# Kernel tuning notes

Hardware: AMD Instinct MI355X
Metric: run time of the kernel (lower is better)

The kernel has to match this reference:

```python
import jax, jax.numpy as jnp
import numpy as np

NUM_HEADS = 12
ROPE_THETA = 10000.0


def rope_angles(hd, end_x, end_y):
    # axial 2D rope angles, shape (L, hd//2); first hd//4 from x-coord, next hd//4 from y-coord
    f = 1.0 / (ROPE_THETA ** (np.arange(0, hd, 4)[: hd // 4].astype(np.float32) / hd))
    t = np.arange(end_x * end_y)
    tx = (t % end_x).astype(np.float32)
    ty = (t // end_x).astype(np.float32)
    ang = np.concatenate([np.outer(tx, f), np.outer(ty, f)], axis=-1)
    return jnp.asarray(ang, dtype=jnp.float32)


def apply_rope(q, ang):
    # q: (B, nH, L, hd); complex multiply on adjacent pairs
    cos, sin = jnp.cos(ang), jnp.sin(ang)  # (L, hd//2)
    qr = q.reshape(*q.shape[:-1], -1, 2)
    a, b = qr[..., 0], qr[..., 1]
    return jnp.stack([a * cos - b * sin, a * sin + b * cos], axis=-1).reshape(q.shape)


def setup_inputs() -> dict:
    key = jax.random.key(0)
    ks = jax.random.split(key, 7)
    dim, H, W, B = 768, 32, 32, 8
    hd = dim // NUM_HEADS
    return {
        "x": jax.random.normal(ks[0], (B, H, W, dim), jnp.float32),
        "qkv_w": jax.random.normal(ks[1], (3 * dim, dim), jnp.float32) * 0.02,
        "qkv_b": jax.random.normal(ks[2], (3 * dim,), jnp.float32) * 0.02,
        "proj_w": jax.random.normal(ks[3], (dim, dim), jnp.float32) * 0.02,
        "proj_b": jax.random.normal(ks[4], (dim,), jnp.float32) * 0.02,
        "rel_pos_h": jax.random.normal(ks[5], (2 * H - 1, hd), jnp.float32) * 0.02,
        "rel_pos_w": jax.random.normal(ks[6], (2 * W - 1, hd), jnp.float32) * 0.02,
    }


def reference(x, qkv_w, qkv_b, proj_w, proj_b, rel_pos_h, rel_pos_w):
    B, H, W, dim = x.shape
    nH = NUM_HEADS
    hd = dim // nH
    L = H * W
    qkv = jnp.einsum("blc,dc->bld", x.reshape(B, L, dim), qkv_w) + qkv_b
    qkv = qkv.reshape(B, L, 3, nH, hd)
    q = qkv[:, :, 0].transpose(0, 2, 1, 3)  # (B, nH, L, hd)
    k = qkv[:, :, 1].transpose(0, 2, 1, 3)
    v = qkv[:, :, 2].transpose(0, 2, 1, 3)
    # 2D rope (applied to both q and k)
    ang = rope_angles(hd, H, W)
    q = apply_rope(q, ang)
    k = apply_rope(k, ang)
    # relative position bias: equivalent math of concat_rel_pos(rescale=True) + SDPA
    # effective scores = (q.k)/sqrt(hd) + rel_h + rel_w
    rc = jnp.arange(H)[:, None] - jnp.arange(W)[None, :] + (H - 1)  # (H, W)
    Rh = rel_pos_h[rc]  # (H, K_h, hd)
    Rw = rel_pos_w[rc]  # (W, K_w, hd)
    rq = q.reshape(B, nH, H, W, hd)
    rel_h = jnp.einsum("bnhwc,hkc->bnhwk", rq, Rh)  # (B, nH, H, W, K_h)
    rel_w = jnp.einsum("bnhwc,wkc->bnhwk", rq, Rw)  # (B, nH, H, W, K_w)
    scores = jnp.einsum("bnqc,bnkc->bnqk", q, k) / jnp.sqrt(jnp.float32(hd))
    scores = scores.reshape(B, nH, H, W, H, W) + rel_h[..., :, None] + rel_w[..., None, :]
    attn = jax.nn.softmax(scores.reshape(B, nH, L, L), axis=-1)
    out = jnp.einsum("bnqk,bnkc->bnqc", attn, v)  # (B, nH, L, hd)
    out = out.transpose(0, 2, 1, 3).reshape(B, H, W, dim)
    return jnp.einsum("bhwc,dc->bhwd", out, proj_w) + proj_b
```

## Files before the change

kernel.cpp:

```cpp
#include <hip/hip_runtime.h>


typedef unsigned short u16;
typedef __attribute__((ext_vector_type(8))) __bf16 bf16x8;
typedef __attribute__((ext_vector_type(4))) float f32x4;
typedef __attribute__((address_space(1))) const unsigned int gu32;
typedef __attribute__((address_space(3))) unsigned int lu32;

#define LOG2E 1.4426950408889634f

__device__ __forceinline__ float b2f(u16 u) {
    unsigned int i = ((unsigned int)u) << 16;
    float f; __builtin_memcpy(&f, &i, 4); return f;
}
__device__ __forceinline__ u16 f2b(float f) {
    unsigned int x; __builtin_memcpy(&x, &f, 4);
    x += 0x7fffu + ((x >> 16) & 1u);
    return (u16)(x >> 16);
}

#define LDT 72

__global__ void detect_dtype(const u16* __restrict__ x, int* __restrict__ flag)
{
    if (threadIdx.x == 0 && blockIdx.x == 0) {
        float mx = 0.f;
        for (int i = 0; i < 128; i++) {
            float v = fabsf(b2f(x[i]));
            if (!(v <= 1e30f)) v = 1e30f;
            mx = fmaxf(mx, v);
        }
        *flag = (mx > 1e4f) ? 1 : 0;
    }
}

struct CvtArgs {
    const void* src[7];
    u16*        dst[7];
    int         n[7];
    float       sc[7];
};

__global__ __launch_bounds__(256) void convert_all(CvtArgs a, const int* __restrict__ flag)
{
    const int fl = *flag;
    const int g = blockIdx.x * 256 + threadIdx.x;
    const int stride = gridDim.x * 256;
    #pragma unroll 1
    for (int s = 0; s < 7; s++) {
        const int n = a.n[s];
        const float sc = a.sc[s];
        const float* fs = (const float*)a.src[s];
        const u16*  hs = (const u16*)a.src[s];
        u16* d = a.dst[s];
        for (int i = g; i < n; i += stride) {
            float v = fl ? fs[i] : b2f(hs[i]);
            d[i] = f2b(v * sc);
        }
    }
}

template <int EPI>
__global__ __launch_bounds__(256) void gemm128(
    const u16* __restrict__ A, const u16* __restrict__ Bw,
    const u16* __restrict__ bias, void* __restrict__ Cout,
    const int* __restrict__ flag, u16* __restrict__ qkvT, int N, int K)
{
    __shared__ __align__(16) u16 smem[16384];
    u16* lA = smem;
    u16* lB = smem + 8192;
    u16* ct = smem;
    const int tid = threadIdx.x;
    const int m0 = blockIdx.x * 128, n0 = blockIdx.y * 128;
    const int wave = tid >> 6, lane = tid & 63;
    const int wm = (wave & 1) * 64, wn = (wave >> 1) * 64;
    const int lm = lane & 15, lq = lane >> 4;
    const int srow = lane >> 3;
    const int sgcol = ((lane & 7) ^ (srow & 7)) * 8;
    const int sw0 = (lq ^ (lm & 7)) * 8;
    const int sw1 = ((lq + 4) ^ (lm & 7)) * 8;
    f32x4 acc[4][4] = {};
    for (int k0 = 0; k0 < K; k0 += 64) {
        if (k0) __syncthreads();
        #pragma unroll
        for (int c4 = 0; c4 < 4; c4++) {
            const int c = wave * 4 + c4;
            const int row = c * 8 + srow;
            __builtin_amdgcn_global_load_lds(
                (gu32*)(A + (size_t)(m0 + row) * K + k0 + sgcol),
                (lu32*)&lA[c * 512], 16, 0, 0);
            __builtin_amdgcn_global_load_lds(
                (gu32*)(Bw + (size_t)(n0 + row) * K + k0 + sgcol),
                (lu32*)&lB[c * 512], 16, 0, 0);
        }
        __syncthreads();
        #pragma unroll
        for (int ks = 0; ks < 64; ks += 32) {
            const int sw = ks ? sw1 : sw0;
            bf16x8 af[4], bfr[4];
            #pragma unroll
            for (int i = 0; i < 4; i++) af[i]  = *(const bf16x8*)&lA[(wm + i * 16 + lm) * 64 + sw];
            #pragma unroll
            for (int j = 0; j < 4; j++) bfr[j] = *(const bf16x8*)&lB[(wn + j * 16 + lm) * 64 + sw];
            #pragma unroll
            for (int i = 0; i < 4; i++)
                #pragma unroll
                for (int j = 0; j < 4; j++)
                    acc[i][j] = __builtin_amdgcn_mfma_f32_16x16x32_bf16(af[i], bfr[j], acc[i][j], 0, 0, 0);
        }
    }
    if (EPI == 0) {
        const int fl = *flag;
        #pragma unroll
        for (int j = 0; j < 4; j++) {
            const int n = n0 + wn + j * 16 + lm;
            const float bj = b2f(bias[n]);
            #pragma unroll
            for (int i = 0; i < 4; i++)
                #pragma unroll
                for (int r = 0; r < 4; r++) {
                    const int m = m0 + wm + i * 16 + lq * 4 + r;
                    const float v = acc[i][j][r] + bj;
                    if (fl) ((float*)Cout)[(size_t)m * 768 + n] = v;
                    else    ((u16*)Cout)[(size_t)m * 768 + n] = f2b(v);
                }
        }
    } else {
        const int which = n0 / 768;
        const bool vt = (which == 2);
        __syncthreads();
        #pragma unroll
        for (int j = 0; j < 4; j++) {
            const int nl = wn + j * 16 + lm;
            const int n = n0 + nl;
            const float bj = b2f(bias[n]);
            #pragma unroll
            for (int i = 0; i < 4; i++)
                #pragma unroll
                for (int r = 0; r < 4; r++) {
                    const int ml = wm + i * 16 + lq * 4 + r;
                    const int m = m0 + ml;
                    float v = acc[i][j][r] + bj;
                    const float p = __shfl_xor(v, 1);
                    const int l = m & 1023, d = n & 63;
                    float o = v;
                    if (which < 2) {
                        const int pi = d >> 1, jj = pi & 15;
                        const float coord = (pi < 16) ? (float)(l & 31) : (float)(l >> 5);
                        const float ang = coord * __expf(-(float)jj * 0.5756462732485115f);
                        float sn, cs; __sincosf(ang, &sn, &cs);
                        o = v * cs + ((d & 1) ? p * sn : -(p * sn));
                        if (which == 1) o *= 0.125f * LOG2E;
                    }
                    ct[vt ? nl * 128 + ml : ml * 128 + nl] = f2b(o);
                }
        }
        __syncthreads();
        const size_t HL = (size_t)96 * 1024 * 64;
        const int nh0 = (n0 >> 6) % 12, bb = m0 >> 10, l0 = m0 & 1023;
        if (!vt) {
            #pragma unroll
            for (int pass = 0; pass < 8; pass++) {
                const int chunk = pass * 256 + tid;
                const int run = chunk >> 3, lc = chunk & 7;
                const int ml = run >> 1, h = run & 1;
                u16* gp = qkvT + (size_t)which * HL
                        + ((size_t)(bb * 12 + nh0 + h) * 1024 + l0 + ml) * 64 + lc * 8;
                *(uint4*)gp = *(const uint4*)&ct[ml * 128 + h * 64 + lc * 8];
            }
        } else {
            const int kt0 = l0 >> 6;
            #pragma unroll
            for (int pass = 0; pass < 8; pass++) {
                const int run = pass * 16 + (tid >> 4);
                const int ln = tid & 15;
                const int half = ln >> 3, l8 = ln & 7;
                u16* gp = qkvT + 2 * HL
                        + (size_t)(bb * 12 + nh0 + (run >> 6)) * 65536
                        + (size_t)(kt0 + half) * 4096 + (run & 63) * 64 + l8 * 8;
                *(uint4*)gp = *(const uint4*)&ct[run * 128 + ln * 8];
            }
        }
    }
}

__global__ __launch_bounds__(256) void flash_attn_mfma(
    const u16* __restrict__ qkvT, const u16* __restrict__ relH,
    const u16* __restrict__ relW, u16* __restrict__ outb)
{
    __shared__ __align__(16) u16 ks2[2 * 4096];
    __shared__ __align__(16) u16 vsT[2 * 4096];
    __shared__ __align__(16) u16 qs[64 * LDT];
    __shared__ __align__(16) u16 Th[64 * LDT];
    __shared__ __align__(16) u16 Tw[64 * LDT];
    u16* rel = vsT;
    u16* pT  = qs;

    const int tid = threadIdx.x;
    const int bn = blockIdx.x, q0 = blockIdx.y * 64;
    const size_t HL = (size_t)96 * 1024 * 64;
    const u16* qg  = qkvT + (size_t)bn * 65536 + (size_t)q0 * 64;
    const u16* kgb = qkvT + HL + (size_t)bn * 65536;
    const u16* vgb = qkvT + 2 * HL + (size_t)bn * 65536;

    for (int g = tid; g < 1024; g += 256) {
        int r = g >> 4, c = (g & 15) * 4;
        *(ushort4*)&qs[r * LDT + c] = ((const ushort4*)qg)[g];
    }
    for (int g = tid; g < 1008; g += 256) {
        int r = g >> 4, c = (g & 15) * 4;
        *(ushort4*)&rel[r * 64 + c] = *(const ushort4*)(relH + g * 4);
    }
    if (tid < 16) { ushort4 z = {0, 0, 0, 0}; *(ushort4*)&rel[63 * 64 + tid * 4] = z; }
    __syncthreads();

    const int w = tid >> 6, lane = tid & 63;
    const int lm = lane & 15, lq = lane >> 4;

    const bf16x8 bq0 = *(const bf16x8*)&qs[(w * 16 + lm) * LDT + lq * 8];
    const bf16x8 bq1 = *(const bf16x8*)&qs[(w * 16 + lm) * LDT + 32 + lq * 8];

    {
        f32x4 tacc[4] = {};
        #pragma unroll
        for (int nb = 0; nb < 4; nb++) {
            bf16x8 r0 = *(const bf16x8*)&rel[(nb * 16 + lm) * 64 + lq * 8];
            bf16x8 r1 = *(const bf16x8*)&rel[(nb * 16 + lm) * 64 + 32 + lq * 8];
            tacc[nb] = __builtin_amdgcn_mfma_f32_16x16x32_bf16(bq0, r0, tacc[nb], 0, 0, 0);
            tacc[nb] = __builtin_amdgcn_mfma_f32_16x16x32_bf16(bq1, r1, tacc[nb], 0, 0, 0);
        }
        #pragma unroll
        for (int nb = 0; nb < 4; nb++)
            #pragma unroll
            for (int rr = 0; rr < 4; rr++)
                Th[(w * 16 + lq * 4 + rr) * LDT + nb * 16 + lm] = f2b(tacc[nb][rr]);
    }
    __syncthreads();
    for (int g = tid; g < 1008; g += 256) {
        int r = g >> 4, c = (g & 15) * 4;
        *(ushort4*)&rel[r * 64 + c] = *(const ushort4*)(relW + g * 4);
    }
    if (tid < 16) { ushort4 z = {0, 0, 0, 0}; *(ushort4*)&rel[63 * 64 + tid * 4] = z; }
    __syncthreads();
    {
        f32x4 tacc[4] = {};
        #pragma unroll
        for (int nb = 0; nb < 4; nb++) {
            bf16x8 r0 = *(const bf16x8*)&rel[(nb * 16 + lm) * 64 + lq * 8];
            bf16x8 r1 = *(const bf16x8*)&rel[(nb * 16 + lm) * 64 + 32 + lq * 8];
            tacc[nb] = __builtin_amdgcn_mfma_f32_16x16x32_bf16(bq0, r0, tacc[nb], 0, 0, 0);
            tacc[nb] = __builtin_amdgcn_mfma_f32_16x16x32_bf16(bq1, r1, tacc[nb], 0, 0, 0);
        }
        #pragma unroll
        for (int nb = 0; nb < 4; nb++)
            #pragma unroll
            for (int rr = 0; rr < 4; rr++)
                Tw[(w * 16 + lq * 4 + rr) * LDT + nb * 16 + lm] = f2b(tacc[nb][rr]);
    }
    const int qw = (w & 1) * 16 + lm;
    float rwc[8];
    #pragma unroll
    for (int mb2 = 0; mb2 < 2; mb2++)
        #pragma unroll
        for (int rr = 0; rr < 4; rr++) {
            const int kw = mb2 * 16 + lq * 4 + rr;
            rwc[mb2 * 4 + rr] = b2f(Tw[(w * 16 + lm) * LDT + qw - kw + 31]) - 16.0f;
        }
    const int qh = (q0 >> 5) + (w >= 2 ? 1 : 0);

    const int srow = lane >> 3;
    const int sgcol = ((lane & 7) ^ (srow & 7)) * 8;
    const int sw0 = (lq ^ (lm & 7)) * 8;
    const int sw1 = ((lq + 4) ^ (lm & 7)) * 8;
    float l_acc = 0.f;
    f32x4 oacc[4] = {};

    __syncthreads();
    #pragma unroll
    for (int c4 = 0; c4 < 2; c4++) {
        const int c = w * 2 + c4;
        const int row = c * 8 + srow;
        __builtin_amdgcn_global_load_lds(
            (gu32*)(kgb + row * 64 + sgcol), (lu32*)&ks2[c * 512], 16, 0, 0);
        __builtin_amdgcn_global_load_lds(
            (gu32*)(vgb + row * 64 + sgcol), (lu32*)&vsT[c * 512], 16, 0, 0);
    }

    #pragma unroll 1
    for (int kt = 0; kt < 16; kt++) {
        __syncthreads();
        const int bo = (kt & 1) * 4096;
        if (kt < 15) {
            const int bn1 = ((kt + 1) & 1) * 4096;
            const u16* kp = kgb + (size_t)(kt + 1) * 4096;
            const u16* vp = vgb + (size_t)(kt + 1) * 4096;
            #pragma unroll
            for (int c4 = 0; c4 < 2; c4++) {
                const int c = w * 2 + c4;
                const int row = c * 8 + srow;
                __builtin_amdgcn_global_load_lds(
                    (gu32*)(kp + row * 64 + sgcol), (lu32*)&ks2[bn1 + c * 512], 16, 0, 0);
                __builtin_amdgcn_global_load_lds(
                    (gu32*)(vp + row * 64 + sgcol), (lu32*)&vsT[bn1 + c * 512], 16, 0, 0);
            }
        }
        f32x4 sacc[4];
        #pragma unroll
        for (int mb = 0; mb < 4; mb++) {
            bf16x8 ka0 = *(const bf16x8*)&ks2[bo + (mb * 16 + lm) * 64 + sw0];
            bf16x8 ka1 = *(const bf16x8*)&ks2[bo + (mb * 16 + lm) * 64 + sw1];
            f32x4 s = {};
            s = __builtin_amdgcn_mfma_f32_16x16x32_bf16(ka0, bq0, s, 0, 0, 0);
            s = __builtin_amdgcn_mfma_f32_16x16x32_bf16(ka1, bq1, s, 0, 0, 0);
            sacc[mb] = s;
        }
        const float rh0 = b2f(Th[(w * 16 + lm) * LDT + qh - 2 * kt + 31]);
        const float rh1 = b2f(Th[(w * 16 + lm) * LDT + qh - 2 * kt + 30]);
        #pragma unroll
        for (int mb = 0; mb < 4; mb++) {
            const float rhv = (mb >= 2) ? rh1 : rh0;
            unsigned pk[2];
            #pragma unroll
            for (int h = 0; h < 2; h++) {
                float p0 = exp2f(sacc[mb][2 * h]     + rhv + rwc[(mb & 1) * 4 + 2 * h]);
                float p1 = exp2f(sacc[mb][2 * h + 1] + rhv + rwc[(mb & 1) * 4 + 2 * h + 1]);
                l_acc += p0; l_acc += p1;
                unsigned u0, u1;
                __builtin_memcpy(&u0, &p0, 4); __builtin_memcpy(&u1, &p1, 4);
                pk[h] = __builtin_amdgcn_perm(u1 + 0x8000u, u0 + 0x8000u, 0x07060302u);
            }
            uint2 u = {pk[0], pk[1]};
            *(uint2*)&pT[(w * 16 + lm) * LDT + mb * 16 + lq * 4] = u;
        }
        const bf16x8 pa0 = *(const bf16x8*)&pT[(w * 16 + lm) * LDT + lq * 8];
        const bf16x8 pa1 = *(const bf16x8*)&pT[(w * 16 + lm) * LDT + 32 + lq * 8];
        #pragma unroll
        for (int nb = 0; nb < 4; nb++) {
            bf16x8 vb0 = *(const bf16x8*)&vsT[bo + (nb * 16 + lm) * 64 + sw0];
            bf16x8 vb1 = *(const bf16x8*)&vsT[bo + (nb * 16 + lm) * 64 + sw1];
            oacc[nb] = __builtin_amdgcn_mfma_f32_16x16x32_bf16(pa0, vb0, oacc[nb], 0, 0, 0);
            oacc[nb] = __builtin_amdgcn_mfma_f32_16x16x32_bf16(pa1, vb1, oacc[nb], 0, 0, 0);
        }
    }
    l_acc += __shfl_xor(l_acc, 16);
    l_acc += __shfl_xor(l_acc, 32);
    const float rinv = 1.f / l_acc;
    float rv[4];
    #pragma unroll
    for (int rr = 0; rr < 4; rr++) rv[rr] = __shfl(rinv, lq * 4 + rr);
    const int bb = bn / 12, nh = bn % 12;
    #pragma unroll
    for (int nb = 0; nb < 4; nb++)
        #pragma unroll
        for (int rr = 0; rr < 4; rr++) {
            const int qrow = q0 + w * 16 + lq * 4 + rr;
            const int d = nb * 16 + lm;
            outb[((size_t)(bb * 1024 + qrow)) * 768 + nh * 64 + d] = f2b(oacc[nb][rr] * rv[rr]);
        }
}

extern "C" void kernel_launch(void* const* d_in, const int* in_sizes, int n_in,
                              void* d_out, int out_size, void* d_ws, size_t ws_size,
                              hipStream_t stream)
{
    u16* ws16  = (u16*)d_ws;
    u16* qkvT  = ws16;
    u16* xb    = ws16 + (size_t)18874368;
    u16* attn  = xb;
    const size_t S = 25165824;
    u16* qkvw_b = ws16 + S;
    u16* projw_b = qkvw_b + 1769472;
    u16* qkvb_b = projw_b + 589824;
    u16* projb_b = qkvb_b + 2304;
    u16* relh_b = projb_b + 768;
    u16* relw_b = relh_b + 4032;
    int* flag = (int*)(ws16 + S + 2370432);

    detect_dtype<<<1, 64, 0, stream>>>((const u16*)d_in[0], flag);

    CvtArgs ca;
    ca.src[0] = d_in[0]; ca.dst[0] = xb;      ca.n[0] = 6291456; ca.sc[0] = 1.0f;
    ca.src[1] = d_in[1]; ca.dst[1] = qkvw_b;  ca.n[1] = 1769472; ca.sc[1] = 1.0f;
    ca.src[2] = d_in[3]; ca.dst[2] = projw_b; ca.n[2] = 589824;  ca.sc[2] = 1.0f;
    ca.src[3] = d_in[2]; ca.dst[3] = qkvb_b;  ca.n[3] = 2304;    ca.sc[3] = 1.0f;
    ca.src[4] = d_in[4]; ca.dst[4] = projb_b; ca.n[4] = 768;     ca.sc[4] = 1.0f;
    ca.src[5] = d_in[5]; ca.dst[5] = relh_b;  ca.n[5] = 4032;    ca.sc[5] = LOG2E;
    ca.src[6] = d_in[6]; ca.dst[6] = relw_b;  ca.n[6] = 4032;    ca.sc[6] = LOG2E;
    convert_all<<<2048, 256, 0, stream>>>(ca, flag);

    gemm128<1><<<dim3(64, 18), 256, 0, stream>>>(xb, qkvw_b, qkvb_b, nullptr, flag, qkvT, 2304, 768);
    flash_attn_mfma<<<dim3(96, 16), 256, 0, stream>>>(qkvT, relh_b, relw_b, attn);
    gemm128<0><<<dim3(64, 6), 256, 0, stream>>>(attn, projw_b, projb_b, d_out, flag, nullptr, 768, 768);
}
```

Measured before the change: 248.6 us.

## Compute softmax row sums via MFMA with ones and swizzle P/Q LDS layout

```diff
diff --git a/kernel.cpp b/kernel.cpp
--- a/kernel.cpp
+++ b/kernel.cpp
@@ -190,22 +190,30 @@
 {
     __shared__ __align__(16) u16 ks2[2 * 4096];
     __shared__ __align__(16) u16 vsT[2 * 4096];
-    __shared__ __align__(16) u16 qs[64 * LDT];
-    __shared__ __align__(16) u16 Th[64 * LDT];
-    __shared__ __align__(16) u16 Tw[64 * LDT];
+    __shared__ __align__(16) u16 pq[4096];
+    __shared__ __align__(16) u16 ThL[64 * 66];
     u16* rel = vsT;
-    u16* pT  = qs;
 
     const int tid = threadIdx.x;
+    const int w = tid >> 6, lane = tid & 63;
+    const int lm = lane & 15, lq = lane >> 4;
+    const int srow = lane >> 3;
+    const int sgcol = ((lane & 7) ^ (srow & 7)) * 8;
+    const int sw0 = (lq ^ (lm & 7)) * 8;
+    const int sw1 = ((lq + 4) ^ (lm & 7)) * 8;
+
     const int bn = blockIdx.x, q0 = blockIdx.y * 64;
     const size_t HL = (size_t)96 * 1024 * 64;
     const u16* qg  = qkvT + (size_t)bn * 65536 + (size_t)q0 * 64;
     const u16* kgb = qkvT + HL + (size_t)bn * 65536;
     const u16* vgb = qkvT + 2 * HL + (size_t)bn * 65536;
 
-    for (int g = tid; g < 1024; g += 256) {
-        int r = g >> 4, c = (g & 15) * 4;
-        *(ushort4*)&qs[r * LDT + c] = ((const ushort4*)qg)[g];
+    #pragma unroll
+    for (int c4 = 0; c4 < 2; c4++) {
+        const int c = w * 2 + c4;
+        const int row = c * 8 + srow;
+        __builtin_amdgcn_global_load_lds(
+            (gu32*)(qg + row * 64 + sgcol), (lu32*)&pq[c * 512], 16, 0, 0);
     }
     for (int g = tid; g < 1008; g += 256) {
         int r = g >> 4, c = (g & 15) * 4;
@@ -214,11 +222,8 @@
     if (tid < 16) { ushort4 z = {0, 0, 0, 0}; *(ushort4*)&rel[63 * 64 + tid * 4] = z; }
     __syncthreads();
 
-    const int w = tid >> 6, lane = tid & 63;
-    const int lm = lane & 15, lq = lane >> 4;
-
-    const bf16x8 bq0 = *(const bf16x8*)&qs[(w * 16 + lm) * LDT + lq * 8];
-    const bf16x8 bq1 = *(const bf16x8*)&qs[(w * 16 + lm) * LDT + 32 + lq * 8];
+    const bf16x8 bq0 = *(const bf16x8*)&pq[(w * 16 + lm) * 64 + sw0];
+    const bf16x8 bq1 = *(const bf16x8*)&pq[(w * 16 + lm) * 64 + sw1];
 
     {
         f32x4 tacc[4] = {};
@@ -233,7 +238,7 @@
         for (int nb = 0; nb < 4; nb++)
             #pragma unroll
             for (int rr = 0; rr < 4; rr++)
-                Th[(w * 16 + lq * 4 + rr) * LDT + nb * 16 + lm] = f2b(tacc[nb][rr]);
+                ThL[(w * 16 + lq * 4 + rr) * 66 + nb * 16 + lm] = f2b(tacc[nb][rr]);
     }
     __syncthreads();
     for (int g = tid; g < 1008; g += 256) {
@@ -255,8 +260,9 @@
         for (int nb = 0; nb < 4; nb++)
             #pragma unroll
             for (int rr = 0; rr < 4; rr++)
-                Tw[(w * 16 + lq * 4 + rr) * LDT + nb * 16 + lm] = f2b(tacc[nb][rr]);
-    }
+                ks2[(w * 16 + lq * 4 + rr) * 66 + nb * 16 + lm] = f2b(tacc[nb][rr]);
+    }
+    __syncthreads();
     const int qw = (w & 1) * 16 + lm;
     float rwc[8];
     #pragma unroll
@@ -264,15 +270,15 @@
         #pragma unroll
         for (int rr = 0; rr < 4; rr++) {
             const int kw = mb2 * 16 + lq * 4 + rr;
-            rwc[mb2 * 4 + rr] = b2f(Tw[(w * 16 + lm) * LDT + qw - kw + 31]) - 16.0f;
+            rwc[mb2 * 4 + rr] = b2f(ks2[(w * 16 + lm) * 66 + qw - kw + 31]) - 16.0f;
         }
     const int qh = (q0 >> 5) + (w >= 2 ? 1 : 0);
 
-    const int srow = lane >> 3;
-    const int sgcol = ((lane & 7) ^ (srow & 7)) * 8;
-    const int sw0 = (lq ^ (lm & 7)) * 8;
-    const int sw1 = ((lq + 4) ^ (lm & 7)) * 8;
-    float l_acc = 0.f;
+    union { unsigned u[4]; bf16x8 v; } uo;
+    uo.u[0] = uo.u[1] = uo.u[2] = uo.u[3] = 0x3F803F80u;
+    const bf16x8 vone = uo.v;
+
+    f32x4 lacc = {};
     f32x4 oacc[4] = {};
 
     __syncthreads();
@@ -314,26 +320,26 @@
             s = __builtin_amdgcn_mfma_f32_16x16x32_bf16(ka1, bq1, s, 0, 0, 0);
             sacc[mb] = s;
         }
-        const float rh0 = b2f(Th[(w * 16 + lm) * LDT + qh - 2 * kt + 31]);
-        const float rh1 = b2f(Th[(w * 16 + lm) * LDT + qh - 2 * kt + 30]);
+        const float rh0 = b2f(ThL[(w * 16 + lm) * 66 + qh - 2 * kt + 31]);
+        const float rh1 = b2f(ThL[(w * 16 + lm) * 66 + qh - 2 * kt + 30]);
         #pragma unroll
         for (int mb = 0; mb < 4; mb++) {
             const float rhv = (mb >= 2) ? rh1 : rh0;
-            unsigned pk[2];
-            #pragma unroll
-            for (int h = 0; h < 2; h++) {
-                float p0 = exp2f(sacc[mb][2 * h]     + rhv + rwc[(mb & 1) * 4 + 2 * h]);
-                float p1 = exp2f(sacc[mb][2 * h + 1] + rhv + rwc[(mb & 1) * 4 + 2 * h + 1]);
-                l_acc += p0; l_acc += p1;
-                unsigned u0, u1;
-                __builtin_memcpy(&u0, &p0, 4); __builtin_memcpy(&u1, &p1, 4);
-                pk[h] = __builtin_amdgcn_perm(u1 + 0x8000u, u0 + 0x8000u, 0x07060302u);
-            }
-            uint2 u = {pk[0], pk[1]};
-            *(uint2*)&pT[(w * 16 + lm) * LDT + mb * 16 + lq * 4] = u;
-        }
-        const bf16x8 pa0 = *(const bf16x8*)&pT[(w * 16 + lm) * LDT + lq * 8];
-        const bf16x8 pa1 = *(const bf16x8*)&pT[(w * 16 + lm) * LDT + 32 + lq * 8];
+            float p0 = exp2f(sacc[mb][0] + rhv + rwc[(mb & 1) * 4 + 0]);
+            float p1 = exp2f(sacc[mb][1] + rhv + rwc[(mb & 1) * 4 + 1]);
+            float p2 = exp2f(sacc[mb][2] + rhv + rwc[(mb & 1) * 4 + 2]);
+            float p3 = exp2f(sacc[mb][3] + rhv + rwc[(mb & 1) * 4 + 3]);
+            unsigned w0, w1;
+            asm("v_cvt_pk_bf16_f32 %0, %1, %2" : "=v"(w0) : "v"(p0), "v"(p1));
+            asm("v_cvt_pk_bf16_f32 %0, %1, %2" : "=v"(w1) : "v"(p2), "v"(p3));
+            uint2 u; u.x = w0; u.y = w1;
+            const int gg = 2 * mb + (lq >> 1);
+            *(uint2*)&pq[(w * 16 + lm) * 64 + ((gg ^ (lm & 7)) * 8) + (lq & 1) * 4] = u;
+        }
+        const bf16x8 pa0 = *(const bf16x8*)&pq[(w * 16 + lm) * 64 + sw0];
+        const bf16x8 pa1 = *(const bf16x8*)&pq[(w * 16 + lm) * 64 + sw1];
+        lacc = __builtin_amdgcn_mfma_f32_16x16x32_bf16(pa0, vone, lacc, 0, 0, 0);
+        lacc = __builtin_amdgcn_mfma_f32_16x16x32_bf16(pa1, vone, lacc, 0, 0, 0);
         #pragma unroll
         for (int nb = 0; nb < 4; nb++) {
             bf16x8 vb0 = *(const bf16x8*)&vsT[bo + (nb * 16 + lm) * 64 + sw0];
@@ -342,12 +348,9 @@
             oacc[nb] = __builtin_amdgcn_mfma_f32_16x16x32_bf16(pa1, vb1, oacc[nb], 0, 0, 0);
         }
     }
-    l_acc += __shfl_xor(l_acc, 16);
-    l_acc += __shfl_xor(l_acc, 32);
-    const float rinv = 1.f / l_acc;
     float rv[4];
     #pragma unroll
-    for (int rr = 0; rr < 4; rr++) rv[rr] = __shfl(rinv, lq * 4 + rr);
+    for (int rr = 0; rr < 4; rr++) rv[rr] = 1.f / lacc[rr];
     const int bb = bn / 12, nh = bn % 12;
     #pragma unroll
     for (int nb = 0; nb < 4; nb++)
```

New measurement: 233.7 us. 6.0% less time.
